# Kernel optimization log

Measured on AMD Instinct MI355X. Metric: run time of the kernel, lower is better.

## Reference

```python
import jax, jax.numpy as jnp
import numpy as np
import math

B, N, F = 32, 1024, 64      # batch, nodes, input_dim (data_size)
PRE = 64                     # preweight (== input_dim so output Linear works)
L1 = 128                     # layer_1


def setup_inputs() -> dict:
    key = jax.random.key(0)
    ks = jax.random.split(key, 12)
    def lin(k, out_d, in_d):
        bound = 1.0 / math.sqrt(in_d)
        kw, kb = jax.random.split(k)
        W = jax.random.uniform(kw, (out_d, in_d), jnp.float32, -bound, bound)
        b = jax.random.uniform(kb, (out_d,), jnp.float32, -bound, bound)
        return W, b
    W_pre, b_pre = lin(ks[0], PRE, F)
    W_fc1, b_fc1 = lin(ks[1], L1, PRE)
    W_keys, b_keys = lin(ks[2], 1, L1)
    W_out, b_out = lin(ks[3], 1, F)
    alpha = jax.random.uniform(ks[4], (1,), jnp.float32)
    x = jax.random.normal(ks[5], (B, N, F), jnp.float32)
    adjacency_matrix = jax.random.uniform(ks[6], (B, N, N), jnp.float32)
    return {
        "x": x, "adjacency_matrix": adjacency_matrix, "alpha": alpha,
        "W_pre": W_pre, "b_pre": b_pre, "W_fc1": W_fc1, "b_fc1": b_fc1,
        "W_keys": W_keys, "b_keys": b_keys, "W_out": W_out, "b_out": b_out,
    }


def reference(x, adjacency_matrix, alpha, W_pre, b_pre, W_fc1, b_fc1,
              W_keys, b_keys, W_out, b_out):
    # --- D^-1/2 A D^-1/2 normalization (D is diagonal -> row/col scaling) ---
    deg = adjacency_matrix.sum(axis=-1)                       # [B, N]
    deg = jnp.where(deg != 0, deg, 1.0)
    d_isqrt = deg ** -0.5                                     # [B, N]
    A_norm = d_isqrt[:, :, None] * adjacency_matrix * d_isqrt[:, None, :]
    # --- (alpha*I + A_norm) @ x ---
    h = alpha[0] * x + jnp.einsum('bij,bjf->bif', A_norm, x)  # [B, N, F]
    # --- node embedding (pre_weighting + relu) ---
    values = jax.nn.relu(h @ W_pre.T + b_pre)                 # [B, N, PRE]
    # --- attention pooling (dropout is identity at eval) ---
    queries = jax.nn.relu(values @ W_fc1.T + b_fc1)           # [B, N, L1]
    logits = (queries @ W_keys.T + b_keys)[..., 0]            # [B, N]
    scores = jax.nn.softmax(logits / math.sqrt(2.0), axis=-1) # [B, N]
    vect = jnp.einsum('bn,bnp->bp', scores, values)           # [B, PRE]
    y = vect @ W_out.T + b_out                                # [B, 1]
    return y
```

## Files before the change

### kernel.cpp

```cpp
#include <hip/hip_runtime.h>


#define N_ 1024
#define F_ 64

typedef short s16x8 __attribute__((ext_vector_type(8)));
typedef float f32x4 __attribute__((ext_vector_type(4)));
typedef unsigned short u16x4 __attribute__((ext_vector_type(4)));
typedef unsigned short u16x8 __attribute__((ext_vector_type(8)));

__device__ __forceinline__ unsigned short bf16rne(float f) {
  union { float f; unsigned u; } v; v.f = f;
  unsigned r = v.u + 0x7fffu + ((v.u >> 16) & 1u);
  return (unsigned short)(r >> 16);
}

__device__ __forceinline__ void fma_row(float (&a)[4], const float4 av,
                                        const float4 x0, const float4 x1,
                                        const float4 x2, const float4 x3) {
  a[0] += av.x * x0.x + av.y * x1.x + av.z * x2.x + av.w * x3.x;
  a[1] += av.x * x0.y + av.y * x1.y + av.z * x2.y + av.w * x3.y;
  a[2] += av.x * x0.z + av.y * x1.z + av.z * x2.z + av.w * x3.z;
  a[3] += av.x * x0.w + av.y * x1.w + av.z * x2.w + av.w * x3.w;
}

__global__ __launch_bounds__(256) void k_prep(const float* __restrict__ A,
                                              float* __restrict__ disq,
                                              unsigned short* __restrict__ Abf) {
  const int row  = blockIdx.x * 4 + (threadIdx.x >> 6);
  const int lane = threadIdx.x & 63;
  const float4* a4 = (const float4*)(A + (size_t)row * N_);
  unsigned short* ob = Abf + (size_t)row * N_;
  float s = 0.f;
#pragma unroll
  for (int it = 0; it < 4; ++it) {
    float4 v = a4[it * 64 + lane];
    s += v.x + v.y + v.z + v.w;
    u16x4 o;
    o[0] = bf16rne(v.x); o[1] = bf16rne(v.y);
    o[2] = bf16rne(v.z); o[3] = bf16rne(v.w);
    *(u16x4*)(ob + (it * 64 + lane) * 4) = o;
  }
#pragma unroll
  for (int off = 32; off > 0; off >>= 1) s += __shfl_down(s, off, 64);
  if (lane == 0) {
    float d = (s != 0.f) ? s : 1.f;
    disq[row] = rsqrtf(d);
  }
}

__global__ __launch_bounds__(256) void k_xt(const float* __restrict__ x,
                                            const float* __restrict__ disq,
                                            unsigned short* __restrict__ xtb) {
  __shared__ float xs[64][68];
  const int b = blockIdx.y, j0 = blockIdx.x * 64, t = threadIdx.x;
  const float* xb = x + ((size_t)b << 16);
  const float* dq = disq + (b << 10);
#pragma unroll
  for (int it = 0; it < 4; ++it) {
    int idx = it * 1024 + t * 4;
    int jj = idx >> 6, ff = idx & 63;
    float4 vv = *(const float4*)&xb[(size_t)(j0 + jj) * F_ + ff];
    float sc = dq[j0 + jj];
    vv.x *= sc; vv.y *= sc; vv.z *= sc; vv.w *= sc;
    *(float4*)&xs[jj][ff] = vv;
  }
  __syncthreads();
  const int f = t & 63, ch = t >> 6;
  u16x8 o0, o1;
#pragma unroll
  for (int jj = 0; jj < 8; ++jj) o0[jj] = bf16rne(xs[ch * 16 + jj][f]);
#pragma unroll
  for (int jj = 0; jj < 8; ++jj) o1[jj] = bf16rne(xs[ch * 16 + 8 + jj][f]);
  unsigned short* dst = xtb + (size_t)(b * 64 + f) * N_ + j0 + ch * 16;
  *(u16x8*)dst = o0;
  *(u16x8*)(dst + 8) = o1;
}

__global__ __launch_bounds__(256) void k_spmm_mlp(const unsigned short* __restrict__ Abf,
                                                  const unsigned short* __restrict__ xtb,
                                                  const float* __restrict__ x,
                                                  const float* __restrict__ disq,
                                                  const float* __restrict__ alphap,
                                                  const float* __restrict__ Wpre,
                                                  const float* __restrict__ bpre,
                                                  const float* __restrict__ Wfc1,
                                                  const float* __restrict__ bfc1,
                                                  const float* __restrict__ Wkeys,
                                                  const float* __restrict__ bkeysp,
                                                  float* __restrict__ values,
                                                  float* __restrict__ logits) {
  __shared__ __attribute__((aligned(16))) char smem[54528];
  float (*hs)[68]   = (float(*)[68])(smem);
  float (*wft)[128] = (float(*)[128])(smem + 17408);
  float (*part)[17] = (float(*)[17])(smem + 50176);

  const int t  = threadIdx.x;
  const int b  = blockIdx.x;
  const int i0 = blockIdx.y * 64;
  const int w  = t >> 6, l = t & 63;
  const int lr = l & 15, kq = l >> 4;

  const int ar0 = t >> 3;
  const int ac0 = t & 7;
  const int ar1 = ar0 + 32;
  const unsigned short* Asrc0 = Abf + ((size_t)b << 20) + (size_t)(i0 + ar0) * N_ + ac0 * 8;
  const unsigned short* Asrc1 = Abf + ((size_t)b << 20) + (size_t)(i0 + ar1) * N_ + ac0 * 8;
  const unsigned short* Bsrc0 = xtb + (size_t)(b * 64 + ar0) * N_ + ac0 * 8;
  const unsigned short* Bsrc1 = xtb + (size_t)(b * 64 + ar1) * N_ + ac0 * 8;
  const int dst0 = ar0 * 128 + ((ac0 ^ (ar0 & 7)) << 4);
  const int dst1 = ar1 * 128 + ((ac0 ^ (ar0 & 7)) << 4);

  {
    s16x8 ra0 = *(const s16x8*)Asrc0;
    s16x8 ra1 = *(const s16x8*)Asrc1;
    s16x8 rb0 = *(const s16x8*)Bsrc0;
    s16x8 rb1 = *(const s16x8*)Bsrc1;
    *(s16x8*)(smem + dst0) = ra0;
    *(s16x8*)(smem + dst1) = ra1;
    *(s16x8*)(smem + 8192 + dst0) = rb0;
    *(s16x8*)(smem + 8192 + dst1) = rb1;
  }
  __syncthreads();

  f32x4 acc0 = {0.f, 0.f, 0.f, 0.f}, acc1 = acc0, acc2 = acc0, acc3 = acc0;
  const int arow = w * 16 + lr;
  const int sw = (lr & 7) << 4;
  int cur = 0;

  for (int ks = 0; ks < 16; ++ks) {
    s16x8 na0, na1, nb0, nb1;
    if (ks < 15) {
      const int ko = (ks + 1) * 64;
      na0 = *(const s16x8*)(Asrc0 + ko);
      na1 = *(const s16x8*)(Asrc1 + ko);
      nb0 = *(const s16x8*)(Bsrc0 + ko);
      nb1 = *(const s16x8*)(Bsrc1 + ko);
    }
    const char* cb = smem + cur * 16384;
#pragma unroll
    for (int s = 0; s < 2; ++s) {
      const int ch = ((kq + 4 * s) << 4);
      s16x8 af = *(const s16x8*)(cb + arow * 128 + (ch ^ sw));
      s16x8 b0 = *(const s16x8*)(cb + 8192 + (0 * 16 + lr) * 128 + (ch ^ sw));
      s16x8 b1 = *(const s16x8*)(cb + 8192 + (1 * 16 + lr) * 128 + (ch ^ sw));
      s16x8 b2 = *(const s16x8*)(cb + 8192 + (2 * 16 + lr) * 128 + (ch ^ sw));
      s16x8 b3 = *(const s16x8*)(cb + 8192 + (3 * 16 + lr) * 128 + (ch ^ sw));
      acc0 = __builtin_amdgcn_mfma_f32_16x16x32_bf16(af, b0, acc0, 0, 0, 0);
      acc1 = __builtin_amdgcn_mfma_f32_16x16x32_bf16(af, b1, acc1, 0, 0, 0);
      acc2 = __builtin_amdgcn_mfma_f32_16x16x32_bf16(af, b2, acc2, 0, 0, 0);
      acc3 = __builtin_amdgcn_mfma_f32_16x16x32_bf16(af, b3, acc3, 0, 0, 0);
    }
    if (ks < 15) {
      char* nbuf = smem + (cur ^ 1) * 16384;
      *(s16x8*)(nbuf + dst0) = na0;
      *(s16x8*)(nbuf + dst1) = na1;
      *(s16x8*)(nbuf + 8192 + dst0) = nb0;
      *(s16x8*)(nbuf + 8192 + dst1) = nb1;
    }
    __syncthreads();
    cur ^= 1;
  }

  const float alpha = alphap[0];
  const float* dq = disq + (b << 10);
  const float* xb = x + ((size_t)b << 16);
  const int rl = w * 16 + kq * 4;
#pragma unroll
  for (int r = 0; r < 4; ++r) {
    float di = dq[i0 + rl + r];
    size_t ro = (size_t)(i0 + rl + r) * F_;
    hs[rl + r][0  + lr] = alpha * xb[ro + 0  + lr] + di * acc0[r];
    hs[rl + r][16 + lr] = alpha * xb[ro + 16 + lr] + di * acc1[r];
    hs[rl + r][32 + lr] = alpha * xb[ro + 32 + lr] + di * acc2[r];
    hs[rl + r][48 + lr] = alpha * xb[ro + 48 + lr] + di * acc3[r];
  }
#pragma unroll
  for (int it = 0; it < 4; ++it) {
    int idx = it * 1024 + t * 4;
    float4 wv = *(const float4*)&Wpre[idx];
    int p = idx >> 6, f = idx & 63;
    wft[f + 0][p] = wv.x; wft[f + 1][p] = wv.y; wft[f + 2][p] = wv.z; wft[f + 3][p] = wv.w;
  }
  __syncthreads();

  const size_t base = ((size_t)(b * 16 + blockIdx.y)) * 4096;
  const int cg = t & 15, rg = t >> 4;
  float acc[4][4] = {{0.f}};
#pragma unroll
  for (int q = 0; q < 16; ++q) {
    float4 xv0 = *(float4*)&wft[q * 4 + 0][cg * 4];
    float4 xv1 = *(float4*)&wft[q * 4 + 1][cg * 4];
    float4 xv2 = *(float4*)&wft[q * 4 + 2][cg * 4];
    float4 xv3 = *(float4*)&wft[q * 4 + 3][cg * 4];
#pragma unroll
    for (int k = 0; k < 4; ++k) {
      float4 av = *(float4*)&hs[rg * 4 + k][q * 4];
      fma_row(acc[k], av, xv0, xv1, xv2, xv3);
    }
  }
  float4 bp = *(const float4*)&bpre[cg * 4];
  __syncthreads();
#pragma unroll
  for (int k = 0; k < 4; ++k) {
    float4 o;
    o.x = fmaxf(acc[k][0] + bp.x, 0.f);
    o.y = fmaxf(acc[k][1] + bp.y, 0.f);
    o.z = fmaxf(acc[k][2] + bp.z, 0.f);
    o.w = fmaxf(acc[k][3] + bp.w, 0.f);
    *(float4*)&hs[rg * 4 + k][cg * 4] = o;
    *(float4*)&values[base + (size_t)(rg * 4 + k) * 64 + cg * 4] = o;
  }
#pragma unroll
  for (int it = 0; it < 8; ++it) {
    int idx = it * 1024 + t * 4;
    int ll = idx >> 6, p = idx & 63;
    float4 wv = *(const float4*)&Wfc1[idx];
    wft[p + 0][ll] = wv.x; wft[p + 1][ll] = wv.y; wft[p + 2][ll] = wv.z; wft[p + 3][ll] = wv.w;
  }
  __syncthreads();

  const int lg = cg;
  float acc_a[4][4] = {{0.f}};
  float acc_b[4][4] = {{0.f}};
#pragma unroll
  for (int q = 0; q < 16; ++q) {
    float4 w0a = *(float4*)&wft[q * 4 + 0][lg * 8];
    float4 w0b = *(float4*)&wft[q * 4 + 0][lg * 8 + 4];
    float4 w1a = *(float4*)&wft[q * 4 + 1][lg * 8];
    float4 w1b = *(float4*)&wft[q * 4 + 1][lg * 8 + 4];
    float4 w2a = *(float4*)&wft[q * 4 + 2][lg * 8];
    float4 w2b = *(float4*)&wft[q * 4 + 2][lg * 8 + 4];
    float4 w3a = *(float4*)&wft[q * 4 + 3][lg * 8];
    float4 w3b = *(float4*)&wft[q * 4 + 3][lg * 8 + 4];
#pragma unroll
    for (int k = 0; k < 4; ++k) {
      float4 vv = *(float4*)&hs[rg * 4 + k][q * 4];
      fma_row(acc_a[k], vv, w0a, w1a, w2a, w3a);
      fma_row(acc_b[k], vv, w0b, w1b, w2b, w3b);
    }
  }
  float4 bfa = *(const float4*)&bfc1[lg * 8];
  float4 bfb = *(const float4*)&bfc1[lg * 8 + 4];
  float4 wka = *(const float4*)&Wkeys[lg * 8];
  float4 wkb = *(const float4*)&Wkeys[lg * 8 + 4];
#pragma unroll
  for (int k = 0; k < 4; ++k) {
    float lp = 0.f;
    lp += fmaxf(acc_a[k][0] + bfa.x, 0.f) * wka.x;
    lp += fmaxf(acc_a[k][1] + bfa.y, 0.f) * wka.y;
    lp += fmaxf(acc_a[k][2] + bfa.z, 0.f) * wka.z;
    lp += fmaxf(acc_a[k][3] + bfa.w, 0.f) * wka.w;
    lp += fmaxf(acc_b[k][0] + bfb.x, 0.f) * wkb.x;
    lp += fmaxf(acc_b[k][1] + bfb.y, 0.f) * wkb.y;
    lp += fmaxf(acc_b[k][2] + bfb.z, 0.f) * wkb.z;
    lp += fmaxf(acc_b[k][3] + bfb.w, 0.f) * wkb.w;
    part[rg * 4 + k][lg] = lp;
  }
  __syncthreads();
  if (t < 64) {
    float s = bkeysp[0];
#pragma unroll
    for (int g = 0; g < 16; ++g) s += part[t][g];
    logits[(b * 16 + blockIdx.y) * 64 + t] = s;
  }
}

__global__ __launch_bounds__(1024) void k_tail(const float* __restrict__ logits,
                                               const float* __restrict__ values,
                                               const float* __restrict__ Wout,
                                               const float* __restrict__ boutp,
                                               float* __restrict__ y) {
  const int b = blockIdx.x, t = threadIdx.x;
  __shared__ float sc[1024];
  __shared__ float red[16];
  __shared__ float pool[16][64];
  const float isq2 = 0.70710678118654752f;
  float lv = logits[(b << 10) + t] * isq2;
  float m = lv;
#pragma unroll
  for (int off = 32; off > 0; off >>= 1) m = fmaxf(m, __shfl_xor(m, off, 64));
  if ((t & 63) == 0) red[t >> 6] = m;
  __syncthreads();
  m = red[0];
#pragma unroll
  for (int i = 1; i < 16; ++i) m = fmaxf(m, red[i]);
  float e = expf(lv - m);
  float s = e;
#pragma unroll
  for (int off = 32; off > 0; off >>= 1) s += __shfl_xor(s, off, 64);
  __syncthreads();
  if ((t & 63) == 0) red[t >> 6] = s;
  __syncthreads();
  s = red[0];
#pragma unroll
  for (int i = 1; i < 16; ++i) s += red[i];
  sc[t] = e * (1.f / s);
  __syncthreads();
  const int c = t & 63, g = t >> 6;
  const float* vb = values + ((size_t)b << 16);
  float acc = 0.f;
#pragma unroll 8
  for (int k = 0; k < 64; ++k) {
    int n = g + 16 * k;
    acc += sc[n] * vb[(size_t)n * 64 + c];
  }
  pool[g][c] = acc;
  __syncthreads();
  if (t < 64) {
    float v = 0.f;
#pragma unroll
    for (int gg = 0; gg < 16; ++gg) v += pool[gg][t];
    float p = v * Wout[t];
#pragma unroll
    for (int off = 32; off > 0; off >>= 1) p += __shfl_down(p, off, 64);
    if (t == 0) y[b] = p + boutp[0];
  }
}

extern "C" void kernel_launch(void* const* d_in, const int* in_sizes, int n_in,
                              void* d_out, int out_size, void* d_ws, size_t ws_size,
                              hipStream_t stream) {
  const float* x     = (const float*)d_in[0];
  const float* A     = (const float*)d_in[1];
  const float* alpha = (const float*)d_in[2];
  const float* Wpre  = (const float*)d_in[3];
  const float* bpre  = (const float*)d_in[4];
  const float* Wfc1  = (const float*)d_in[5];
  const float* bfc1  = (const float*)d_in[6];
  const float* Wkeys = (const float*)d_in[7];
  const float* bkeys = (const float*)d_in[8];
  const float* Wout  = (const float*)d_in[9];
  const float* bout  = (const float*)d_in[10];
  float* y = (float*)d_out;

  float* ws     = (float*)d_ws;
  float* disq   = ws;
  float* values = disq + 32768;
  float* logits = values + 2097152;
  unsigned short* xtb = (unsigned short*)(logits + 32768);
  unsigned short* Abf = xtb + 2097152;

  k_prep    <<<dim3(8192),   dim3(256),  0, stream>>>(A, disq, Abf);
  k_xt      <<<dim3(16, 32), dim3(256),  0, stream>>>(x, disq, xtb);
  k_spmm_mlp<<<dim3(32, 16), dim3(256),  0, stream>>>(Abf, xtb, x, disq, alpha,
                                                      Wpre, bpre, Wfc1, bfc1, Wkeys, bkeys,
                                                      values, logits);
  k_tail    <<<dim3(32),     dim3(1024), 0, stream>>>(logits, values, Wout, bout, y);
}
```

Before: 78.85 us.

## Deepen SpMM prefetch, split tail pooling across blocks, nontemporal A loads

The A-to-bf16 prep kernel now reads A with nontemporal loads so the streamed fp32 adjacency matrix does not pollute the cache. The SpMM main loop prefetches global tiles two steps ahead and writes the next LDS buffer before the MFMAs instead of after, which should hide more global latency. The tail softmax-pooling kernel is split into 8 chunks per batch (256 blocks instead of 32), followed by a small reduction kernel. The split adds a launch, and each tail block recomputes the full softmax redundantly.

Result: slower. 81.36 us (+3.2%).

```diff
diff --git a/kernel.cpp b/kernel.cpp
--- a/kernel.cpp
+++ b/kernel.cpp
@@ -29,16 +29,16 @@
                                               unsigned short* __restrict__ Abf) {
   const int row  = blockIdx.x * 4 + (threadIdx.x >> 6);
   const int lane = threadIdx.x & 63;
-  const float4* a4 = (const float4*)(A + (size_t)row * N_);
+  const f32x4* a4 = (const f32x4*)(A + (size_t)row * N_);
   unsigned short* ob = Abf + (size_t)row * N_;
   float s = 0.f;
 #pragma unroll
   for (int it = 0; it < 4; ++it) {
-    float4 v = a4[it * 64 + lane];
-    s += v.x + v.y + v.z + v.w;
+    f32x4 v = __builtin_nontemporal_load(a4 + it * 64 + lane);
+    s += v[0] + v[1] + v[2] + v[3];
     u16x4 o;
-    o[0] = bf16rne(v.x); o[1] = bf16rne(v.y);
-    o[2] = bf16rne(v.z); o[3] = bf16rne(v.w);
+    o[0] = bf16rne(v[0]); o[1] = bf16rne(v[1]);
+    o[2] = bf16rne(v[2]); o[3] = bf16rne(v[3]);
     *(u16x4*)(ob + (it * 64 + lane) * 4) = o;
   }
 #pragma unroll
@@ -111,15 +111,22 @@
   const int dst0 = ar0 * 128 + ((ac0 ^ (ar0 & 7)) << 4);
   const int dst1 = ar1 * 128 + ((ac0 ^ (ar0 & 7)) << 4);
 
+  s16x8 wa0, wa1, wb0, wb1;
+  s16x8 la0, la1, lb0, lb1;
+
   {
-    s16x8 ra0 = *(const s16x8*)Asrc0;
-    s16x8 ra1 = *(const s16x8*)Asrc1;
-    s16x8 rb0 = *(const s16x8*)Bsrc0;
-    s16x8 rb1 = *(const s16x8*)Bsrc1;
-    *(s16x8*)(smem + dst0) = ra0;
-    *(s16x8*)(smem + dst1) = ra1;
-    *(s16x8*)(smem + 8192 + dst0) = rb0;
-    *(s16x8*)(smem + 8192 + dst1) = rb1;
+    s16x8 a0 = *(const s16x8*)Asrc0;
+    s16x8 a1 = *(const s16x8*)Asrc1;
+    s16x8 b0 = *(const s16x8*)Bsrc0;
+    s16x8 b1 = *(const s16x8*)Bsrc1;
+    *(s16x8*)(smem + dst0) = a0;
+    *(s16x8*)(smem + dst1) = a1;
+    *(s16x8*)(smem + 8192 + dst0) = b0;
+    *(s16x8*)(smem + 8192 + dst1) = b1;
+    wa0 = *(const s16x8*)(Asrc0 + 64);
+    wa1 = *(const s16x8*)(Asrc1 + 64);
+    wb0 = *(const s16x8*)(Bsrc0 + 64);
+    wb1 = *(const s16x8*)(Bsrc1 + 64);
   }
   __syncthreads();
 
@@ -129,13 +136,19 @@
   int cur = 0;
 
   for (int ks = 0; ks < 16; ++ks) {
-    s16x8 na0, na1, nb0, nb1;
+    if (ks < 14) {
+      const int ko = (ks + 2) * 64;
+      la0 = *(const s16x8*)(Asrc0 + ko);
+      la1 = *(const s16x8*)(Asrc1 + ko);
+      lb0 = *(const s16x8*)(Bsrc0 + ko);
+      lb1 = *(const s16x8*)(Bsrc1 + ko);
+    }
     if (ks < 15) {
-      const int ko = (ks + 1) * 64;
-      na0 = *(const s16x8*)(Asrc0 + ko);
-      na1 = *(const s16x8*)(Asrc1 + ko);
-      nb0 = *(const s16x8*)(Bsrc0 + ko);
-      nb1 = *(const s16x8*)(Bsrc1 + ko);
+      char* nbuf = smem + (cur ^ 1) * 16384;
+      *(s16x8*)(nbuf + dst0) = wa0;
+      *(s16x8*)(nbuf + dst1) = wa1;
+      *(s16x8*)(nbuf + 8192 + dst0) = wb0;
+      *(s16x8*)(nbuf + 8192 + dst1) = wb1;
     }
     const char* cb = smem + cur * 16384;
 #pragma unroll
@@ -151,13 +164,7 @@
       acc2 = __builtin_amdgcn_mfma_f32_16x16x32_bf16(af, b2, acc2, 0, 0, 0);
       acc3 = __builtin_amdgcn_mfma_f32_16x16x32_bf16(af, b3, acc3, 0, 0, 0);
     }
-    if (ks < 15) {
-      char* nbuf = smem + (cur ^ 1) * 16384;
-      *(s16x8*)(nbuf + dst0) = na0;
-      *(s16x8*)(nbuf + dst1) = na1;
-      *(s16x8*)(nbuf + 8192 + dst0) = nb0;
-      *(s16x8*)(nbuf + 8192 + dst1) = nb1;
-    }
+    if (ks < 14) { wa0 = la0; wa1 = la1; wb0 = lb0; wb1 = lb1; }
     __syncthreads();
     cur ^= 1;
   }
@@ -268,10 +275,8 @@
 
 __global__ __launch_bounds__(1024) void k_tail(const float* __restrict__ logits,
                                                const float* __restrict__ values,
-                                               const float* __restrict__ Wout,
-                                               const float* __restrict__ boutp,
-                                               float* __restrict__ y) {
-  const int b = blockIdx.x, t = threadIdx.x;
+                                               float* __restrict__ vpart) {
+  const int c = blockIdx.x, b = blockIdx.y, t = threadIdx.x;
   __shared__ float sc[1024];
   __shared__ float red[16];
   __shared__ float pool[16][64];
@@ -297,24 +302,39 @@
   for (int i = 1; i < 16; ++i) s += red[i];
   sc[t] = e * (1.f / s);
   __syncthreads();
-  const int c = t & 63, g = t >> 6;
+  const int col = t & 63, g = t >> 6;
   const float* vb = values + ((size_t)b << 16);
   float acc = 0.f;
-#pragma unroll 8
-  for (int k = 0; k < 64; ++k) {
-    int n = g + 16 * k;
-    acc += sc[n] * vb[(size_t)n * 64 + c];
-  }
-  pool[g][c] = acc;
+#pragma unroll
+  for (int k = 0; k < 8; ++k) {
+    int n = c * 128 + g + 16 * k;
+    acc += sc[n] * vb[(size_t)n * 64 + col];
+  }
+  pool[g][col] = acc;
   __syncthreads();
   if (t < 64) {
     float v = 0.f;
 #pragma unroll
     for (int gg = 0; gg < 16; ++gg) v += pool[gg][t];
-    float p = v * Wout[t];
+    vpart[(b * 8 + c) * 64 + t] = v;
+  }
+}
+
+__global__ __launch_bounds__(256) void k_out(const float* __restrict__ vpart,
+                                             const float* __restrict__ Wout,
+                                             const float* __restrict__ boutp,
+                                             float* __restrict__ y) {
+  const int t = threadIdx.x, w = t >> 6, lane = t & 63;
+#pragma unroll
+  for (int it = 0; it < 8; ++it) {
+    int b = w * 8 + it;
+    float v = 0.f;
+#pragma unroll
+    for (int ch = 0; ch < 8; ++ch) v += vpart[(b * 8 + ch) * 64 + lane];
+    float p = v * Wout[lane];
 #pragma unroll
     for (int off = 32; off > 0; off >>= 1) p += __shfl_down(p, off, 64);
-    if (t == 0) y[b] = p + boutp[0];
+    if (lane == 0) y[b] = p + boutp[0];
   }
 }
 
@@ -338,7 +358,8 @@
   float* disq   = ws;
   float* values = disq + 32768;
   float* logits = values + 2097152;
-  unsigned short* xtb = (unsigned short*)(logits + 32768);
+  float* vpart  = logits + 32768;
+  unsigned short* xtb = (unsigned short*)(vpart + 16384);
   unsigned short* Abf = xtb + 2097152;
 
   k_prep    <<<dim3(8192),   dim3(256),  0, stream>>>(A, disq, Abf);
@@ -346,5 +367,6 @@
   k_spmm_mlp<<<dim3(32, 16), dim3(256),  0, stream>>>(Abf, xtb, x, disq, alpha,
                                                       Wpre, bpre, Wfc1, bfc1, Wkeys, bkeys,
                                                       values, logits);
-  k_tail    <<<dim3(32),     dim3(1024), 0, stream>>>(logits, values, Wout, bout, y);
-}
+  k_tail    <<<dim3(8, 32),  dim3(1024), 0, stream>>>(logits, values, vpart);
+  k_out     <<<dim3(1),      dim3(256),  0, stream>>>(vpart, Wout, bout, y);
+}
```
